# Performance work log

Hardware: AMD Instinct MI355X
Metric: run time of the kernel (lower is better)

Reference implementation:

```python
import jax, jax.numpy as jnp
import numpy as np

D_MODEL = 1024
SCALE = float(np.sqrt(D_MODEL))


def setup_inputs() -> dict:
    key = jax.random.key(0)
    k1, k2, k3 = jax.random.split(key, 3)
    input_data = jax.random.normal(k1, (4, 2048, D_MODEL), dtype=jnp.float32)
    qk = jax.random.normal(k2, (D_MODEL, D_MODEL), dtype=jnp.float32) / SCALE
    ov = jax.random.normal(k3, (D_MODEL, D_MODEL), dtype=jnp.float32) / SCALE
    return {"input_data": input_data, "qk": qk, "ov": ov}


def reference(input_data, qk, ov):
    # input_data: [B, S, D]; qk, ov: [D, D]
    S = input_data.shape[1]
    # scores: [B, S, S] = (x @ qk) @ x^T / sqrt(D)
    scores = jnp.einsum("bsd,de,bte->bst", input_data, qk, input_data) / SCALE
    # causal mask: positions t > s get -inf (upper triangle, diagonal=1)
    causal = jnp.tril(jnp.ones((S, S), dtype=bool))
    scores = jnp.where(causal, scores, -jnp.inf)
    attn = jax.nn.softmax(scores, axis=-1)
    # A: [B, S, D] = attn @ x @ ov
    return jnp.einsum("bst,btd,de->bse", attn, input_data, ov)
```

## Files before the change

### kernel.cpp

```cpp
#include <hip/hip_runtime.h>
#include <hip/hip_bf16.h>
#include <cstdint>
#include <cstddef>
#include <type_traits>


using bf16 = __hip_bfloat16;
typedef __attribute__((ext_vector_type(8))) short short8;
typedef __attribute__((ext_vector_type(4))) float f32x4;

#define NB 4
#define SS 2048
#define DD 1024

__device__ __forceinline__ void async_lds16(const bf16* g, bf16* l) {
  __builtin_amdgcn_global_load_lds(
      (const __attribute__((address_space(1))) void*)g,
      (__attribute__((address_space(3))) void*)l,
      16, 0, 0);
}

struct alignas(8) bf16x4s { bf16 a, b, c, d; };

__global__ __launch_bounds__(256) void prep_kernel(const float* __restrict__ x,
                                                   bf16* __restrict__ xb,
                                                   const float* __restrict__ qk,
                                                   bf16* __restrict__ qkT,
                                                   const float* __restrict__ ov,
                                                   bf16* __restrict__ ovT,
                                                   float* __restrict__ l) {
  __shared__ bf16 tile[64][65];
  const int bx = blockIdx.x;
  if (bx < 8192) {
    int i = (bx * 256 + threadIdx.x) * 4;
    float4 v = *(const float4*)(x + i);
    bf16x4s o{__float2bfloat16(v.x), __float2bfloat16(v.y),
              __float2bfloat16(v.z), __float2bfloat16(v.w)};
    *(bf16x4s*)(xb + i) = o;
  } else if (bx < 8704) {
    const int idx = bx - 8192;
    const float* in = (idx & 256) ? ov : qk;
    bf16* out = (idx & 256) ? ovT : qkT;
    const int rem = idx & 255;
    const int tbx = (rem & 15) * 64;
    const int tby = (rem >> 4) * 64;
    const int tc = threadIdx.x & 63;
    const int tr = threadIdx.x >> 6;
#pragma unroll
    for (int r = tr; r < 64; r += 4)
      tile[tc][r] = __float2bfloat16(in[(size_t)(tby + r) * DD + tbx + tc]);
    __syncthreads();
#pragma unroll
    for (int r = tr; r < 64; r += 4)
      out[(size_t)(tbx + r) * DD + tby + tc] = tile[r][tc];
  } else {
    const int t = (bx - 8704) * 256 + threadIdx.x;
    f32x4 z = {0.f, 0.f, 0.f, 0.f};
    *(f32x4*)(l + t * 4) = z;
  }
}

__device__ __forceinline__ void gemm256_core(const bf16* __restrict__ Ab,
                                             const bf16* __restrict__ Bb,
                                             bf16* __restrict__ C,
                                             int N, int K, int m0, int n0, int nk,
                                             bf16* As, bf16* Bs) {
  const int lane = threadIdx.x & 63;
  const int wave = threadIdx.x >> 6;
  const int wr   = wave >> 2;
  const int wc   = wave & 3;
  const int quad = lane >> 4;
  const int r    = lane & 15;

  f32x4 acc[8][4];
#pragma unroll
  for (int i = 0; i < 8; ++i)
#pragma unroll
    for (int n = 0; n < 4; ++n) acc[i][n] = f32x4{0.f, 0.f, 0.f, 0.f};

  const int lrow = lane >> 3;
  const int lsw  = (lane & 7) ^ lrow;
  const long long a_lane = (long long)(m0 + wave * 8 + lrow) * K + lsw * 8;
  const long long b_lane = (long long)(n0 + wave * 8 + lrow) * K + lsw * 8;

  auto stageA = [&](int kt, int rnd, int buf) {
    async_lds16(Ab + a_lane + (long long)(rnd * 64) * K + (long long)kt * 64,
                As + buf * 16384 + (rnd * 64 + wave * 8) * 64);
  };
  auto stageB = [&](int kt, int rnd, int buf) {
    async_lds16(Bb + b_lane + (long long)(rnd * 64) * K + (long long)kt * 64,
                Bs + buf * 16384 + (rnd * 64 + wave * 8) * 64);
  };

  stageA(0, 0, 0); stageA(0, 2, 0);
  stageB(0, 0, 0); stageB(0, 1, 0); stageB(0, 2, 0); stageB(0, 3, 0);
  stageA(0, 1, 0); stageA(0, 3, 0);
  asm volatile("s_waitcnt vmcnt(2)" ::: "memory");
  asm volatile("s_barrier" ::: "memory");

  const int ca0 = (quad ^ (r & 7)) * 8;
  const int ca1 = ((4 + quad) ^ (r & 7)) * 8;

  for (int kt = 0; kt < nk; ++kt) {
    const int buf = kt & 1, nxt = buf ^ 1;
    const bool hn = (kt + 1 < nk);
    const bf16* Abuf = As + buf * 16384 + (wr * 128) * 64;
    const bf16* Bbuf = Bs + buf * 16384 + (wc * 64) * 64;

    auto phase = [&](auto RHC, int ca, auto&& stg, int wmode) {
      constexpr int RH = decltype(RHC)::value;
      short8 af[4], bfr[4];
#pragma unroll
      for (int m = 0; m < 4; ++m)
        af[m] = *(const short8*)(Abuf + (RH * 64 + m * 16 + r) * 64 + ca);
#pragma unroll
      for (int n = 0; n < 4; ++n)
        bfr[n] = *(const short8*)(Bbuf + (n * 16 + r) * 64 + ca);
      stg();
      asm volatile("s_barrier" ::: "memory");
      asm volatile("s_waitcnt lgkmcnt(0)" ::: "memory");
      __builtin_amdgcn_sched_barrier(0);
      __builtin_amdgcn_s_setprio(1);
#pragma unroll
      for (int m = 0; m < 4; ++m)
#pragma unroll
        for (int n = 0; n < 4; ++n)
          acc[RH * 4 + m][n] = __builtin_amdgcn_mfma_f32_16x16x32_bf16(
              af[m], bfr[n], acc[RH * 4 + m][n], 0, 0, 0);
      __builtin_amdgcn_s_setprio(0);
      if (wmode == 1) {
        if (hn) asm volatile("s_waitcnt vmcnt(2)" ::: "memory");
        else    asm volatile("s_waitcnt vmcnt(0)" ::: "memory");
      } else if (wmode == 2) {
        if (hn) asm volatile("s_waitcnt vmcnt(2)" ::: "memory");
      }
      asm volatile("s_barrier" ::: "memory");
    };

    phase(std::integral_constant<int, 0>{}, ca0,
          [&] { if (hn) { stageA(kt + 1, 0, nxt); stageA(kt + 1, 2, nxt); } }, 1);
    phase(std::integral_constant<int, 1>{}, ca0,
          [&] { if (hn) { stageB(kt + 1, 0, nxt); stageB(kt + 1, 1, nxt); } }, 0);
    phase(std::integral_constant<int, 0>{}, ca1,
          [&] { if (hn) { stageB(kt + 1, 2, nxt); stageB(kt + 1, 3, nxt); } }, 0);
    phase(std::integral_constant<int, 1>{}, ca1,
          [&] { if (hn) { stageA(kt + 1, 1, nxt); stageA(kt + 1, 3, nxt); } }, 2);
  }

#pragma unroll
  for (int i = 0; i < 8; ++i) {
    const int row0 = m0 + wr * 128 + i * 16 + quad * 4;
#pragma unroll
    for (int n = 0; n < 4; ++n) {
      const int col = n0 + wc * 64 + n * 16 + r;
#pragma unroll
      for (int q = 0; q < 4; ++q)
        C[(long long)(row0 + q) * N + col] = __float2bfloat16(acc[i][n][q]);
    }
  }
}

__device__ __forceinline__ void gemm64_sc(const bf16* __restrict__ Ab,
                                          const bf16* __restrict__ Bb,
                                          bf16* __restrict__ P,
                                          float* __restrict__ l,
                                          int N, int K, int m0, int n0, int nk,
                                          bf16* As, bf16* Bs) {
  const int lane = threadIdx.x & 63;
  const int wave = threadIdx.x >> 6;
  const int wm   = (wave >> 1) * 32;
  const int wn   = (wave & 1) * 64;
  const int quad = lane >> 4;
  const int r    = lane & 15;

  f32x4 acc[2][4];
#pragma unroll
  for (int m = 0; m < 2; ++m)
#pragma unroll
    for (int n = 0; n < 4; ++n) acc[m][n] = f32x4{0.f, 0.f, 0.f, 0.f};

  const int lrow = lane >> 3;
  const int lsw  = (lane & 7) ^ lrow;
  const long long a_lane = (long long)(m0 + lrow) * K + lsw * 8;
  const long long b_lane = (long long)(n0 + lrow) * K + lsw * 8;

  auto stageA = [&](int kt, int rnd, int buf) {
    async_lds16(Ab + a_lane + (long long)(rnd * 32 + wave * 8) * K + (long long)kt * 64,
                As + buf * 4096 + (rnd * 32 + wave * 8) * 64);
  };
  auto stageB = [&](int kt, int rnd, int buf) {
    async_lds16(Bb + b_lane + (long long)(rnd * 32 + wave * 8) * K + (long long)kt * 64,
                Bs + buf * 8192 + (rnd * 32 + wave * 8) * 64);
  };

  stageA(0, 0, 0); stageA(0, 1, 0);
  stageB(0, 0, 0); stageB(0, 1, 0); stageB(0, 2, 0); stageB(0, 3, 0);
  asm volatile("s_waitcnt vmcnt(0)" ::: "memory");
  asm volatile("s_barrier" ::: "memory");

  const int ca0 = (quad ^ (r & 7)) * 8;
  const int ca1 = ((4 + quad) ^ (r & 7)) * 8;

  for (int kt = 0; kt < nk; ++kt) {
    const int buf = kt & 1, nxt = buf ^ 1;
    const bool hn = (kt + 1 < nk);
    const bf16* Abuf = As + buf * 4096;
    const bf16* Bbuf = Bs + buf * 8192;

    auto phase = [&](int ca, auto&& stg, bool tail) {
      short8 af[2], bfr[4];
#pragma unroll
      for (int m = 0; m < 2; ++m)
        af[m] = *(const short8*)(Abuf + (wm + m * 16 + r) * 64 + ca);
#pragma unroll
      for (int n = 0; n < 4; ++n)
        bfr[n] = *(const short8*)(Bbuf + (wn + n * 16 + r) * 64 + ca);
      stg();
      asm volatile("s_barrier" ::: "memory");
      asm volatile("s_waitcnt lgkmcnt(0)" ::: "memory");
      __builtin_amdgcn_sched_barrier(0);
      __builtin_amdgcn_s_setprio(1);
#pragma unroll
      for (int m = 0; m < 2; ++m)
#pragma unroll
        for (int n = 0; n < 4; ++n)
          acc[m][n] = __builtin_amdgcn_mfma_f32_16x16x32_bf16(
              af[m], bfr[n], acc[m][n], 0, 0, 0);
      __builtin_amdgcn_s_setprio(0);
      if (tail && hn) asm volatile("s_waitcnt vmcnt(0)" ::: "memory");
      asm volatile("s_barrier" ::: "memory");
    };

    phase(ca0, [&] { if (hn) { stageA(kt + 1, 0, nxt); stageA(kt + 1, 1, nxt);
                               stageB(kt + 1, 0, nxt); } }, false);
    phase(ca1, [&] { if (hn) { stageB(kt + 1, 1, nxt); stageB(kt + 1, 2, nxt);
                               stageB(kt + 1, 3, nxt); } }, true);
  }

#pragma unroll
  for (int m = 0; m < 2; ++m) {
    const int row0 = m0 + wm + m * 16 + quad * 4;
    float qs[4] = {0.f, 0.f, 0.f, 0.f};
#pragma unroll
    for (int n = 0; n < 4; ++n) {
      const int col = n0 + wn + n * 16 + r;
#pragma unroll
      for (int q = 0; q < 4; ++q) {
        const int row = row0 + q;
        float v = (col <= row) ? __expf(acc[m][n][q] * 0.03125f) : 0.0f;
        P[(long long)row * N + col] = __float2bfloat16(v);
        qs[q] += v;
      }
    }
#pragma unroll
    for (int q = 0; q < 4; ++q) {
#pragma unroll
      for (int off = 1; off < 16; off <<= 1) qs[q] += __shfl_xor(qs[q], off, 64);
      if (r == 0) atomicAdd(&l[row0 + q], qs[q]);
    }
  }
}

__device__ __forceinline__ void gemm128_pv(const bf16* __restrict__ Ab,
                                           const bf16* __restrict__ Bb,
                                           float* __restrict__ C,
                                           const float* __restrict__ l,
                                           int N, int K, int m0, int n0, int nk,
                                           bf16* As, bf16* Bs) {
  const int lane = threadIdx.x & 63;
  const int wave = threadIdx.x >> 6;
  const int wr   = wave >> 1;
  const int wc   = wave & 1;
  const int quad = lane >> 4;
  const int r    = lane & 15;

  f32x4 acc[4][4];
#pragma unroll
  for (int m = 0; m < 4; ++m)
#pragma unroll
    for (int n = 0; n < 4; ++n) acc[m][n] = f32x4{0.f, 0.f, 0.f, 0.f};

  const int lrow = lane >> 3;
  const int lsw  = (lane & 7) ^ lrow;
  const long long a_base = (long long)(m0 + wave * 32 + lrow) * K + lsw * 8;
  const long long b_base = (long long)(n0 + wave * 32 + lrow) * K + lsw * 8;

  auto stageA = [&](int kt, int buf) {
#pragma unroll
    for (int i = 0; i < 4; ++i)
      async_lds16(Ab + a_base + (long long)(i * 8) * K + (long long)kt * 64,
                  As + buf * 8192 + (wave * 32 + i * 8) * 64);
  };
  auto stageB = [&](int kt, int buf) {
#pragma unroll
    for (int i = 0; i < 4; ++i)
      async_lds16(Bb + b_base + (long long)(i * 8) * K + (long long)kt * 64,
                  Bs + buf * 8192 + (wave * 32 + i * 8) * 64);
  };

  stageB(0, 0); stageA(0, 0); stageA(1, 1);
  asm volatile("s_waitcnt vmcnt(4)" ::: "memory");
  asm volatile("s_barrier" ::: "memory");

  const int ca0 = (quad ^ (r & 7)) * 8;
  const int ca1 = ((4 + quad) ^ (r & 7)) * 8;

  int ba = 0;
  for (int kt = 0; kt < nk; ++kt) {
    const int bb = kt & 1;
    int ba2 = ba + 2; if (ba2 >= 3) ba2 -= 3;
    const bool hA = (kt + 2 < nk), hB = (kt + 1 < nk);
    const bf16* Abuf = As + ba * 8192;
    const bf16* Bbuf = Bs + bb * 8192;

    auto phase = [&](int ca, auto&& stg, bool tail) {
      short8 af[4], bfr[4];
#pragma unroll
      for (int m = 0; m < 4; ++m)
        af[m] = *(const short8*)(Abuf + (wr * 64 + m * 16 + r) * 64 + ca);
#pragma unroll
      for (int n = 0; n < 4; ++n)
        bfr[n] = *(const short8*)(Bbuf + (wc * 64 + n * 16 + r) * 64 + ca);
      stg();
      asm volatile("s_barrier" ::: "memory");
      asm volatile("s_waitcnt lgkmcnt(0)" ::: "memory");
      __builtin_amdgcn_sched_barrier(0);
      __builtin_amdgcn_s_setprio(1);
#pragma unroll
      for (int m = 0; m < 4; ++m)
#pragma unroll
        for (int n = 0; n < 4; ++n)
          acc[m][n] = __builtin_amdgcn_mfma_f32_16x16x32_bf16(
              af[m], bfr[n], acc[m][n], 0, 0, 0);
      __builtin_amdgcn_s_setprio(0);
      if (tail) {
        if (hA)      asm volatile("s_waitcnt vmcnt(4)" ::: "memory");
        else if (hB) asm volatile("s_waitcnt vmcnt(0)" ::: "memory");
      }
      asm volatile("s_barrier" ::: "memory");
    };

    phase(ca0, [&] { if (hB) stageB(kt + 1, bb ^ 1);
                     if (hA) stageA(kt + 2, ba2); }, false);
    phase(ca1, [&] {}, true);

    if (++ba == 3) ba = 0;
  }

#pragma unroll
  for (int m = 0; m < 4; ++m) {
    const int row0 = m0 + wr * 64 + m * 16 + quad * 4;
    float rs[4];
#pragma unroll
    for (int q = 0; q < 4; ++q) rs[q] = 1.0f / l[row0 + q];
#pragma unroll
    for (int n = 0; n < 4; ++n) {
      const int col = n0 + wc * 64 + n * 16 + r;
#pragma unroll
      for (int q = 0; q < 4; ++q)
        C[(long long)(row0 + q) * N + col] = acc[m][n][q] * rs[q];
    }
  }
}

__global__ __launch_bounds__(512, 2) void gemm_qv256(const bf16* __restrict__ xb,
                                                     const bf16* __restrict__ qkT,
                                                     const bf16* __restrict__ ovT,
                                                     bf16* __restrict__ Qb,
                                                     bf16* __restrict__ Vt) {
  extern __shared__ bf16 lds[];
  bf16* As = lds;
  bf16* Bs = lds + 32768;
  const long long SD = (long long)SS * DD;
  const int z = blockIdx.z;
  if (z < 4) {
    const int bn = blockIdx.x & 3, bm = blockIdx.x >> 2;
    gemm256_core(xb + z * SD, qkT, Qb + z * SD, DD, DD, bm * 256, bn * 256, 16, As, Bs);
  } else {
    const int bm = blockIdx.x & 3, bn = blockIdx.x >> 2;
    gemm256_core(ovT, xb + (z - 4) * SD, Vt + (z - 4) * SD, SS, DD, bm * 256, bn * 256, 16, As, Bs);
  }
}

__global__ __launch_bounds__(256, 3) void gemm_sc64(const bf16* __restrict__ Qb,
                                                    const bf16* __restrict__ xb,
                                                    bf16* __restrict__ P,
                                                    float* __restrict__ l) {
  extern __shared__ bf16 lds[];
  bf16* As = lds;
  bf16* Bs = lds + 8192;
  const long long SD = (long long)SS * DD;
  const long long SSQ = (long long)SS * SS;
  const int t = blockIdx.x;
  int k = (int)((sqrtf(4.0f * (float)t + 1.0f) - 1.0f) * 0.5f);
  while ((k + 1) * (k + 2) <= t) ++k;
  while (k * (k + 1) > t) --k;
  int s, c;
  if (t < (k + 1) * (k + 1)) { s = 2 * k;     c = t - k * (k + 1); }
  else                       { s = 2 * k + 1; c = t - (k + 1) * (k + 1); }
  const int b = blockIdx.z;
  gemm64_sc(Qb + b * SD, xb + b * SD, P + b * SSQ, l + b * SS,
            SS, DD, s * 64, c * 128, 16, As, Bs);
}

__global__ __launch_bounds__(256, 2) void gemm_pv128(const bf16* __restrict__ P,
                                                     const bf16* __restrict__ Vt,
                                                     float* __restrict__ l,
                                                     float* __restrict__ out) {
  extern __shared__ bf16 lds[];
  bf16* As = lds;
  bf16* Bs = lds + 24576;
  const long long SD = (long long)SS * DD;
  const long long SSQ = (long long)SS * SS;
  const int c  = blockIdx.x & 7;
  const int pr = blockIdx.x >> 3;
  const int b  = blockIdx.z;
  const int n0 = c * 128;
  const int rL = 15 - pr;
  gemm128_pv(P + b * SSQ, Vt + b * SD, out + b * SD, l + b * SS,
             DD, SS, rL * 128, n0, 2 * (rL + 1), As, Bs);
  __syncthreads();
  gemm128_pv(P + b * SSQ, Vt + b * SD, out + b * SD, l + b * SS,
             DD, SS, pr * 128, n0, 2 * (pr + 1), As, Bs);
}

extern "C" void kernel_launch(void* const* d_in, const int* in_sizes, int n_in,
                              void* d_out, int out_size, void* d_ws, size_t ws_size,
                              hipStream_t stream) {
  const float* x  = (const float*)d_in[0];
  const float* qk = (const float*)d_in[1];
  const float* ov = (const float*)d_in[2];
  float* out = (float*)d_out;

  char* ws = (char*)d_ws;
  const size_t MB = 1ull << 20;
  bf16*  xb  = (bf16*)(ws + 0);
  bf16*  qkT = (bf16*)(ws + 16 * MB);
  bf16*  ovT = (bf16*)(ws + 18 * MB);
  bf16*  Qb  = (bf16*)(ws + 20 * MB);
  bf16*  Vt  = (bf16*)(ws + 36 * MB);
  bf16*  P   = (bf16*)(ws + 52 * MB);
  float* l   = (float*)(ws + 84 * MB);

  static bool lds_opt_in = false;
  if (!lds_opt_in) {
    hipFuncSetAttribute((const void*)gemm_qv256,
                        hipFuncAttributeMaxDynamicSharedMemorySize, 131072);
    hipFuncSetAttribute((const void*)gemm_sc64,
                        hipFuncAttributeMaxDynamicSharedMemorySize, 49152);
    hipFuncSetAttribute((const void*)gemm_pv128,
                        hipFuncAttributeMaxDynamicSharedMemorySize, 81920);
    lds_opt_in = true;
  }

  prep_kernel<<<dim3(8712), 256, 0, stream>>>(x, xb, qk, qkT, ov, ovT, l);
  gemm_qv256<<<dim3(32, 1, 8), 512, 131072, stream>>>(xb, qkT, ovT, Qb, Vt);
  gemm_sc64<<<dim3(272, 1, 4), 256, 49152, stream>>>(Qb, xb, P, l);
  gemm_pv128<<<dim3(64, 1, 4), 256, 81920, stream>>>(P, Vt, l, out);
}
```

Before: 191.8 us.

## Shrink QV GEMM tile to 256x128 with K=32 steps and simpler pipeline

```diff
diff --git a/kernel.cpp b/kernel.cpp
--- a/kernel.cpp
+++ b/kernel.cpp
@@ -60,103 +60,104 @@
   }
 }
 
-__device__ __forceinline__ void gemm256_core(const bf16* __restrict__ Ab,
+__device__ __forceinline__ void gemm_qv_core(const bf16* __restrict__ Ab,
                                              const bf16* __restrict__ Bb,
                                              bf16* __restrict__ C,
                                              int N, int K, int m0, int n0, int nk,
                                              bf16* As, bf16* Bs) {
   const int lane = threadIdx.x & 63;
   const int wave = threadIdx.x >> 6;
-  const int wr   = wave >> 2;
-  const int wc   = wave & 3;
+  const int wm   = (wave >> 1) * 64;
+  const int wn   = (wave & 1) * 64;
   const int quad = lane >> 4;
   const int r    = lane & 15;
 
-  f32x4 acc[8][4];
-#pragma unroll
-  for (int i = 0; i < 8; ++i)
-#pragma unroll
-    for (int n = 0; n < 4; ++n) acc[i][n] = f32x4{0.f, 0.f, 0.f, 0.f};
-
-  const int lrow = lane >> 3;
-  const int lsw  = (lane & 7) ^ lrow;
-  const long long a_lane = (long long)(m0 + wave * 8 + lrow) * K + lsw * 8;
-  const long long b_lane = (long long)(n0 + wave * 8 + lrow) * K + lsw * 8;
-
-  auto stageA = [&](int kt, int rnd, int buf) {
-    async_lds16(Ab + a_lane + (long long)(rnd * 64) * K + (long long)kt * 64,
-                As + buf * 16384 + (rnd * 64 + wave * 8) * 64);
-  };
-  auto stageB = [&](int kt, int rnd, int buf) {
-    async_lds16(Bb + b_lane + (long long)(rnd * 64) * K + (long long)kt * 64,
-                Bs + buf * 16384 + (rnd * 64 + wave * 8) * 64);
-  };
-
-  stageA(0, 0, 0); stageA(0, 2, 0);
-  stageB(0, 0, 0); stageB(0, 1, 0); stageB(0, 2, 0); stageB(0, 3, 0);
-  stageA(0, 1, 0); stageA(0, 3, 0);
-  asm volatile("s_waitcnt vmcnt(2)" ::: "memory");
+  f32x4 acc[4][4];
+#pragma unroll
+  for (int m = 0; m < 4; ++m)
+#pragma unroll
+    for (int n = 0; n < 4; ++n) acc[m][n] = f32x4{0.f, 0.f, 0.f, 0.f};
+
+  const int lrow = lane >> 2;
+  const int lsw  = ((lane & 3) - ((lane >> 3) & 3)) & 3;
+  const long long a_lane = (long long)(m0 + lrow) * K + lsw * 8;
+  const long long b_lane = (long long)(n0 + lrow) * K + lsw * 8;
+
+  auto stageA = [&](int kt, int c, int buf) {
+    async_lds16(Ab + a_lane + (long long)(wave * 32 + c * 16) * K + (long long)kt * 32,
+                As + buf * 8192 + (wave * 32 + c * 16) * 32);
+  };
+  auto stageB = [&](int kt, int buf) {
+    async_lds16(Bb + b_lane + (long long)(wave * 16) * K + (long long)kt * 32,
+                Bs + buf * 4096 + (wave * 16) * 32);
+  };
+
+  stageA(0, 0, 0); stageA(0, 1, 0); stageB(0, 0);
+  asm volatile("s_waitcnt vmcnt(0)" ::: "memory");
   asm volatile("s_barrier" ::: "memory");
 
-  const int ca0 = (quad ^ (r & 7)) * 8;
-  const int ca1 = ((4 + quad) ^ (r & 7)) * 8;
-
-  for (int kt = 0; kt < nk; ++kt) {
-    const int buf = kt & 1, nxt = buf ^ 1;
-    const bool hn = (kt + 1 < nk);
-    const bf16* Abuf = As + buf * 16384 + (wr * 128) * 64;
-    const bf16* Bbuf = Bs + buf * 16384 + (wc * 64) * 64;
-
-    auto phase = [&](auto RHC, int ca, auto&& stg, int wmode) {
-      constexpr int RH = decltype(RHC)::value;
-      short8 af[4], bfr[4];
-#pragma unroll
-      for (int m = 0; m < 4; ++m)
-        af[m] = *(const short8*)(Abuf + (RH * 64 + m * 16 + r) * 64 + ca);
+  const int ca = ((quad + (r >> 1)) & 3) * 8;
+
+  for (int t = 0; t < nk; ++t) {
+    const int buf = t & 1, nxt = buf ^ 1;
+    const bool hn = (t + 1 < nk);
+    const bf16* Abuf = As + buf * 8192;
+    const bf16* Bbuf = Bs + buf * 4096;
+
+    short8 af[4], bfr[4];
+#pragma unroll
+    for (int m = 0; m < 4; ++m)
+      af[m] = *(const short8*)(Abuf + (wm + m * 16 + r) * 32 + ca);
+#pragma unroll
+    for (int n = 0; n < 4; ++n)
+      bfr[n] = *(const short8*)(Bbuf + (wn + n * 16 + r) * 32 + ca);
+
+    if (hn) { stageA(t + 1, 0, nxt); stageA(t + 1, 1, nxt); stageB(t + 1, nxt); }
+
+    asm volatile("s_waitcnt lgkmcnt(0)" ::: "memory");
+    __builtin_amdgcn_sched_barrier(0);
+    __builtin_amdgcn_s_setprio(1);
+#pragma unroll
+    for (int m = 0; m < 4; ++m)
 #pragma unroll
       for (int n = 0; n < 4; ++n)
-        bfr[n] = *(const short8*)(Bbuf + (n * 16 + r) * 64 + ca);
-      stg();
-      asm volatile("s_barrier" ::: "memory");
-      asm volatile("s_waitcnt lgkmcnt(0)" ::: "memory");
-      __builtin_amdgcn_sched_barrier(0);
-      __builtin_amdgcn_s_setprio(1);
-#pragma unroll
-      for (int m = 0; m < 4; ++m)
-#pragma unroll
-        for (int n = 0; n < 4; ++n)
-          acc[RH * 4 + m][n] = __builtin_amdgcn_mfma_f32_16x16x32_bf16(
-              af[m], bfr[n], acc[RH * 4 + m][n], 0, 0, 0);
-      __builtin_amdgcn_s_setprio(0);
-      if (wmode == 1) {
-        if (hn) asm volatile("s_waitcnt vmcnt(2)" ::: "memory");
-        else    asm volatile("s_waitcnt vmcnt(0)" ::: "memory");
-      } else if (wmode == 2) {
-        if (hn) asm volatile("s_waitcnt vmcnt(2)" ::: "memory");
-      }
-      asm volatile("s_barrier" ::: "memory");
-    };
-
-    phase(std::integral_constant<int, 0>{}, ca0,
-          [&] { if (hn) { stageA(kt + 1, 0, nxt); stageA(kt + 1, 2, nxt); } }, 1);
-    phase(std::integral_constant<int, 1>{}, ca0,
-          [&] { if (hn) { stageB(kt + 1, 0, nxt); stageB(kt + 1, 1, nxt); } }, 0);
-    phase(std::integral_constant<int, 0>{}, ca1,
-          [&] { if (hn) { stageB(kt + 1, 2, nxt); stageB(kt + 1, 3, nxt); } }, 0);
-    phase(std::integral_constant<int, 1>{}, ca1,
-          [&] { if (hn) { stageA(kt + 1, 1, nxt); stageA(kt + 1, 3, nxt); } }, 2);
-  }
-
-#pragma unroll
-  for (int i = 0; i < 8; ++i) {
-    const int row0 = m0 + wr * 128 + i * 16 + quad * 4;
+        acc[m][n] = __builtin_amdgcn_mfma_f32_16x16x32_bf16(
+            af[m], bfr[n], acc[m][n], 0, 0, 0);
+    __builtin_amdgcn_s_setprio(0);
+
+    if (hn) asm volatile("s_waitcnt vmcnt(0)" ::: "memory");
+    asm volatile("s_barrier" ::: "memory");
+  }
+
+#pragma unroll
+  for (int m = 0; m < 4; ++m) {
+    const int row0 = m0 + wm + m * 16 + quad * 4;
 #pragma unroll
     for (int n = 0; n < 4; ++n) {
-      const int col = n0 + wc * 64 + n * 16 + r;
+      const int col = n0 + wn + n * 16 + r;
 #pragma unroll
       for (int q = 0; q < 4; ++q)
-        C[(long long)(row0 + q) * N + col] = __float2bfloat16(acc[i][n][q]);
+        C[(long long)(row0 + q) * N + col] = __float2bfloat16(acc[m][n][q]);
     }
+  }
+}
+
+__global__ __launch_bounds__(512, 2) void gemm_qv(const bf16* __restrict__ xb,
+                                                  const bf16* __restrict__ qkT,
+                                                  const bf16* __restrict__ ovT,
+                                                  bf16* __restrict__ Qb,
+                                                  bf16* __restrict__ Vt) {
+  extern __shared__ bf16 lds[];
+  bf16* As = lds;
+  bf16* Bs = lds + 16384;
+  const long long SD = (long long)SS * DD;
+  const int z = blockIdx.z;
+  if (z < 4) {
+    const int bn = blockIdx.x & 7, bm = blockIdx.x >> 3;
+    gemm_qv_core(xb + z * SD, qkT, Qb + z * SD, DD, DD, bm * 256, bn * 128, 32, As, Bs);
+  } else {
+    const int bm = blockIdx.x & 3, bn = blockIdx.x >> 2;
+    gemm_qv_core(ovT, xb + (z - 4) * SD, Vt + (z - 4) * SD, SS, DD, bm * 256, bn * 128, 32, As, Bs);
   }
 }
 
@@ -360,25 +361,6 @@
       for (int q = 0; q < 4; ++q)
         C[(long long)(row0 + q) * N + col] = acc[m][n][q] * rs[q];
     }
-  }
-}
-
-__global__ __launch_bounds__(512, 2) void gemm_qv256(const bf16* __restrict__ xb,
-                                                     const bf16* __restrict__ qkT,
-                                                     const bf16* __restrict__ ovT,
-                                                     bf16* __restrict__ Qb,
-                                                     bf16* __restrict__ Vt) {
-  extern __shared__ bf16 lds[];
-  bf16* As = lds;
-  bf16* Bs = lds + 32768;
-  const long long SD = (long long)SS * DD;
-  const int z = blockIdx.z;
-  if (z < 4) {
-    const int bn = blockIdx.x & 3, bm = blockIdx.x >> 2;
-    gemm256_core(xb + z * SD, qkT, Qb + z * SD, DD, DD, bm * 256, bn * 256, 16, As, Bs);
-  } else {
-    const int bm = blockIdx.x & 3, bn = blockIdx.x >> 2;
-    gemm256_core(ovT, xb + (z - 4) * SD, Vt + (z - 4) * SD, SS, DD, bm * 256, bn * 256, 16, As, Bs);
   }
 }
 
@@ -444,8 +426,8 @@
 
   static bool lds_opt_in = false;
   if (!lds_opt_in) {
-    hipFuncSetAttribute((const void*)gemm_qv256,
-                        hipFuncAttributeMaxDynamicSharedMemorySize, 131072);
+    hipFuncSetAttribute((const void*)gemm_qv,
+                        hipFuncAttributeMaxDynamicSharedMemorySize, 49152);
     hipFuncSetAttribute((const void*)gemm_sc64,
                         hipFuncAttributeMaxDynamicSharedMemorySize, 49152);
     hipFuncSetAttribute((const void*)gemm_pv128,
@@ -454,7 +436,7 @@
   }
 
   prep_kernel<<<dim3(8712), 256, 0, stream>>>(x, xb, qk, qkT, ov, ovT, l);
-  gemm_qv256<<<dim3(32, 1, 8), 512, 131072, stream>>>(xb, qkT, ovT, Qb, Vt);
+  gemm_qv<<<dim3(64, 1, 8), 512, 49152, stream>>>(xb, qkT, ovT, Qb, Vt);
   gemm_sc64<<<dim3(272, 1, 4), 256, 49152, stream>>>(Qb, xb, P, l);
   gemm_pv128<<<dim3(64, 1, 4), 256, 81920, stream>>>(P, Vt, l, out);
 }
```

After: 193.1 us. About the same (+0.7%).

## Triple-buffer A tiles and halve phases per k-step in 256 GEMM

Applied to the files above, without the earlier changes.

```diff
diff --git a/kernel.cpp b/kernel.cpp
--- a/kernel.cpp
+++ b/kernel.cpp
@@ -83,36 +83,44 @@
   const long long a_lane = (long long)(m0 + wave * 8 + lrow) * K + lsw * 8;
   const long long b_lane = (long long)(n0 + wave * 8 + lrow) * K + lsw * 8;
 
-  auto stageA = [&](int kt, int rnd, int buf) {
-    async_lds16(Ab + a_lane + (long long)(rnd * 64) * K + (long long)kt * 64,
-                As + buf * 16384 + (rnd * 64 + wave * 8) * 64);
-  };
-  auto stageB = [&](int kt, int rnd, int buf) {
-    async_lds16(Bb + b_lane + (long long)(rnd * 64) * K + (long long)kt * 64,
-                Bs + buf * 16384 + (rnd * 64 + wave * 8) * 64);
-  };
-
-  stageA(0, 0, 0); stageA(0, 2, 0);
-  stageB(0, 0, 0); stageB(0, 1, 0); stageB(0, 2, 0); stageB(0, 3, 0);
-  stageA(0, 1, 0); stageA(0, 3, 0);
-  asm volatile("s_waitcnt vmcnt(2)" ::: "memory");
+  auto stageA = [&](int kt, int buf) {
+#pragma unroll
+    for (int rnd = 0; rnd < 4; ++rnd)
+      async_lds16(Ab + a_lane + (long long)(rnd * 64) * K + (long long)kt * 64,
+                  As + buf * 16384 + (rnd * 64 + wave * 8) * 64);
+  };
+  auto stageB = [&](int kt, int buf) {
+#pragma unroll
+    for (int rnd = 0; rnd < 4; ++rnd)
+      async_lds16(Bb + b_lane + (long long)(rnd * 64) * K + (long long)kt * 64,
+                  Bs + buf * 16384 + (rnd * 64 + wave * 8) * 64);
+  };
+
+  stageA(0, 0); stageB(0, 0);
+  if (nk > 1) {
+    stageA(1, 1);
+    asm volatile("s_waitcnt vmcnt(4)" ::: "memory");
+  } else {
+    asm volatile("s_waitcnt vmcnt(0)" ::: "memory");
+  }
   asm volatile("s_barrier" ::: "memory");
 
   const int ca0 = (quad ^ (r & 7)) * 8;
   const int ca1 = ((4 + quad) ^ (r & 7)) * 8;
 
+  int ba = 0;
   for (int kt = 0; kt < nk; ++kt) {
-    const int buf = kt & 1, nxt = buf ^ 1;
-    const bool hn = (kt + 1 < nk);
-    const bf16* Abuf = As + buf * 16384 + (wr * 128) * 64;
-    const bf16* Bbuf = Bs + buf * 16384 + (wc * 64) * 64;
-
-    auto phase = [&](auto RHC, int ca, auto&& stg, int wmode) {
-      constexpr int RH = decltype(RHC)::value;
-      short8 af[4], bfr[4];
-#pragma unroll
-      for (int m = 0; m < 4; ++m)
-        af[m] = *(const short8*)(Abuf + (RH * 64 + m * 16 + r) * 64 + ca);
+    const int bb = kt & 1;
+    int ba2 = ba + 2; if (ba2 >= 3) ba2 -= 3;
+    const bool hB = (kt + 1 < nk), hA = (kt + 2 < nk);
+    const bf16* Abuf = As + ba * 16384 + (wr * 128) * 64;
+    const bf16* Bbuf = Bs + bb * 16384 + (wc * 64) * 64;
+
+    auto phase = [&](int ca, auto&& stg, bool tail) {
+      short8 af[8], bfr[4];
+#pragma unroll
+      for (int m = 0; m < 8; ++m)
+        af[m] = *(const short8*)(Abuf + (m * 16 + r) * 64 + ca);
 #pragma unroll
       for (int n = 0; n < 4; ++n)
         bfr[n] = *(const short8*)(Bbuf + (n * 16 + r) * 64 + ca);
@@ -122,29 +130,23 @@
       __builtin_amdgcn_sched_barrier(0);
       __builtin_amdgcn_s_setprio(1);
 #pragma unroll
-      for (int m = 0; m < 4; ++m)
+      for (int m = 0; m < 8; ++m)
 #pragma unroll
         for (int n = 0; n < 4; ++n)
-          acc[RH * 4 + m][n] = __builtin_amdgcn_mfma_f32_16x16x32_bf16(
-              af[m], bfr[n], acc[RH * 4 + m][n], 0, 0, 0);
+          acc[m][n] = __builtin_amdgcn_mfma_f32_16x16x32_bf16(
+              af[m], bfr[n], acc[m][n], 0, 0, 0);
       __builtin_amdgcn_s_setprio(0);
-      if (wmode == 1) {
-        if (hn) asm volatile("s_waitcnt vmcnt(2)" ::: "memory");
-        else    asm volatile("s_waitcnt vmcnt(0)" ::: "memory");
-      } else if (wmode == 2) {
-        if (hn) asm volatile("s_waitcnt vmcnt(2)" ::: "memory");
+      if (tail) {
+        if (hA)      asm volatile("s_waitcnt vmcnt(4)" ::: "memory");
+        else         asm volatile("s_waitcnt vmcnt(0)" ::: "memory");
       }
       asm volatile("s_barrier" ::: "memory");
     };
 
-    phase(std::integral_constant<int, 0>{}, ca0,
-          [&] { if (hn) { stageA(kt + 1, 0, nxt); stageA(kt + 1, 2, nxt); } }, 1);
-    phase(std::integral_constant<int, 1>{}, ca0,
-          [&] { if (hn) { stageB(kt + 1, 0, nxt); stageB(kt + 1, 1, nxt); } }, 0);
-    phase(std::integral_constant<int, 0>{}, ca1,
-          [&] { if (hn) { stageB(kt + 1, 2, nxt); stageB(kt + 1, 3, nxt); } }, 0);
-    phase(std::integral_constant<int, 1>{}, ca1,
-          [&] { if (hn) { stageA(kt + 1, 1, nxt); stageA(kt + 1, 3, nxt); } }, 2);
+    phase(ca0, [&] { if (hB) stageB(kt + 1, bb ^ 1); }, false);
+    phase(ca1, [&] { if (hA) stageA(kt + 2, ba2); }, true);
+
+    if (++ba == 3) ba = 0;
   }
 
 #pragma unroll
@@ -157,6 +159,25 @@
       for (int q = 0; q < 4; ++q)
         C[(long long)(row0 + q) * N + col] = __float2bfloat16(acc[i][n][q]);
     }
+  }
+}
+
+__global__ __launch_bounds__(512, 2) void gemm_qv256(const bf16* __restrict__ xb,
+                                                     const bf16* __restrict__ qkT,
+                                                     const bf16* __restrict__ ovT,
+                                                     bf16* __restrict__ Qb,
+                                                     bf16* __restrict__ Vt) {
+  extern __shared__ bf16 lds[];
+  bf16* As = lds;
+  bf16* Bs = lds + 49152;
+  const long long SD = (long long)SS * DD;
+  const int z = blockIdx.z;
+  if (z < 4) {
+    const int bn = blockIdx.x & 3, bm = blockIdx.x >> 2;
+    gemm256_core(xb + z * SD, qkT, Qb + z * SD, DD, DD, bm * 256, bn * 256, 16, As, Bs);
+  } else {
+    const int bm = blockIdx.x & 3, bn = blockIdx.x >> 2;
+    gemm256_core(ovT, xb + (z - 4) * SD, Vt + (z - 4) * SD, SS, DD, bm * 256, bn * 256, 16, As, Bs);
   }
 }
 
@@ -360,25 +381,6 @@
       for (int q = 0; q < 4; ++q)
         C[(long long)(row0 + q) * N + col] = acc[m][n][q] * rs[q];
     }
-  }
-}
-
-__global__ __launch_bounds__(512, 2) void gemm_qv256(const bf16* __restrict__ xb,
-                                                     const bf16* __restrict__ qkT,
-                                                     const bf16* __restrict__ ovT,
-                                                     bf16* __restrict__ Qb,
-                                                     bf16* __restrict__ Vt) {
-  extern __shared__ bf16 lds[];
-  bf16* As = lds;
-  bf16* Bs = lds + 32768;
-  const long long SD = (long long)SS * DD;
-  const int z = blockIdx.z;
-  if (z < 4) {
-    const int bn = blockIdx.x & 3, bm = blockIdx.x >> 2;
-    gemm256_core(xb + z * SD, qkT, Qb + z * SD, DD, DD, bm * 256, bn * 256, 16, As, Bs);
-  } else {
-    const int bm = blockIdx.x & 3, bn = blockIdx.x >> 2;
-    gemm256_core(ovT, xb + (z - 4) * SD, Vt + (z - 4) * SD, SS, DD, bm * 256, bn * 256, 16, As, Bs);
   }
 }
 
@@ -445,7 +447,7 @@
   static bool lds_opt_in = false;
   if (!lds_opt_in) {
     hipFuncSetAttribute((const void*)gemm_qv256,
-                        hipFuncAttributeMaxDynamicSharedMemorySize, 131072);
+                        hipFuncAttributeMaxDynamicSharedMemorySize, 163840);
     hipFuncSetAttribute((const void*)gemm_sc64,
                         hipFuncAttributeMaxDynamicSharedMemorySize, 49152);
     hipFuncSetAttribute((const void*)gemm_pv128,
@@ -454,7 +456,7 @@
   }
 
   prep_kernel<<<dim3(8712), 256, 0, stream>>>(x, xb, qk, qkT, ov, ovT, l);
-  gemm_qv256<<<dim3(32, 1, 8), 512, 131072, stream>>>(xb, qkT, ovT, Qb, Vt);
+  gemm_qv256<<<dim3(32, 1, 8), 512, 163840, stream>>>(xb, qkT, ovT, Qb, Vt);
   gemm_sc64<<<dim3(272, 1, 4), 256, 49152, stream>>>(Qb, xb, P, l);
   gemm_pv128<<<dim3(64, 1, 4), 256, 81920, stream>>>(P, Vt, l, out);
 }
```

Result: no change. 192.4 us (+0.3%).
